# Optimization experiments

Hardware: AMD Instinct MI355X
Metric: run time of the kernel (lower is better)

The kernel has to match this reference:

```python
import jax, jax.numpy as jnp
import numpy as np

N_EMBED = 192
N_HEAD = 6
HEAD_DIM = N_EMBED // N_HEAD  # 32


def setup_inputs() -> dict:
    key = jax.random.key(0)
    k1, k2, k3, k4, k5 = jax.random.split(key, 5)
    B, T = 2048, 128
    scale_qkv = 1.0 / np.sqrt(N_EMBED)
    return {
        "x": jax.random.normal(k1, (B, T, N_EMBED), dtype=jnp.float32),
        "w_qkv": jax.random.normal(k2, (N_EMBED, 3 * N_EMBED), dtype=jnp.float32) * scale_qkv,
        "b_qkv": jax.random.normal(k3, (3 * N_EMBED,), dtype=jnp.float32) * 0.01,
        "w_proj": jax.random.normal(k4, (N_EMBED, N_EMBED), dtype=jnp.float32) * scale_qkv,
        "b_proj": jax.random.normal(k5, (N_EMBED,), dtype=jnp.float32) * 0.01,
    }


def reference(x, w_qkv, b_qkv, w_proj, b_proj):
    B, T, C = x.shape
    qkv = x @ w_qkv + b_qkv                       # [B, T, 3C]
    q, k, v = jnp.split(qkv, 3, axis=-1)
    # [B, H, T, D]
    def heads(t):
        return t.reshape(B, T, N_HEAD, HEAD_DIM).transpose(0, 2, 1, 3)
    q, k, v = heads(q), heads(k), heads(v)
    att = jnp.einsum("bhtd,bhsd->bhts", q, k) / np.sqrt(HEAD_DIM).astype(x.dtype)
    causal = jnp.tril(jnp.ones((T, T), dtype=bool))
    att = jnp.where(causal, att, jnp.finfo(att.dtype).min)
    att = jax.nn.softmax(att, axis=-1)
    # dropout is identity in eval mode
    y = jnp.einsum("bhts,bhsd->bhtd", att, v)      # [B, H, T, D]
    y = y.transpose(0, 2, 1, 3).reshape(B, T, C)
    return y @ w_proj + b_proj
```

## Files before the change

kernel.cpp:

```cpp
#include <hip/hip_runtime.h>
#include <hip/hip_bf16.h>

#define T_  128
#define C_  192
#define H_  6
#define C3_ 576
#define SLAB_ELEMS (96 * 192)
#define SLAB_BYTES (SLAB_ELEMS * 2)

typedef __bf16 bf16x8 __attribute__((ext_vector_type(8)));
typedef __bf16 bf16x4 __attribute__((ext_vector_type(4)));
typedef float  f32x4  __attribute__((ext_vector_type(4)));
typedef unsigned short u16;

__global__ void prep_weights(const float* __restrict__ w_qkv,
                             const float* __restrict__ w_proj,
                             u16* __restrict__ wt)
{
    int idx = blockIdx.x * 256 + threadIdx.x;
    if (idx >= 8 * SLAB_ELEMS) return;
    int slab = idx / SLAB_ELEMS;
    int rem  = idx % SLAB_ELEMS;
    int nl   = rem / 192;
    int kkp  = rem % 192;
    int d    = kkp ^ ((nl & 7) << 3);
    int kt   = d >> 5;
    int e    = d & 31;
    int g    = e >> 3;
    int r    = e & 7;
    int hi   = r >> 2;
    int i    = r & 3;
    int k    = kt * 32 + hi * 16 + g * 4 + i;
    float v;
    if (slab < 6) {
        int sec = nl >> 5;
        int col = sec * C_ + slab * 32 + (nl & 31);
        v = w_qkv[(size_t)k * C3_ + col];
    } else {
        int col = (slab - 6) * 96 + nl;
        v = w_proj[(size_t)k * C_ + col];
    }
    __bf16 bv = (__bf16)v;
    wt[idx] = *reinterpret_cast<u16*>(&bv);
}

__device__ __forceinline__ bf16x8 ld_frag(const __bf16* p) {
    union { bf16x8 v; struct { bf16x4 lo, hi; } s; } u;
    u.s.lo = *reinterpret_cast<const bf16x4*>(p);
    u.s.hi = *reinterpret_cast<const bf16x4*>(p + 16);
    return u.v;
}

__device__ __forceinline__ bf16x8 ld_w(const __bf16* wl, int nl, int kt, int g) {
    return *reinterpret_cast<const bf16x8*>(
        &wl[nl * 192 + (((kt << 5) + (g << 3)) ^ ((nl & 7) << 3))]);
}

__device__ __forceinline__ void stage_slab(const u16* __restrict__ src, u16* dst,
                                           int wid, int lane) {
    #pragma unroll
    for (int p = 0; p < 9; ++p) {
        int off = p * 2048 + wid * 512;
        __builtin_amdgcn_global_load_lds(
            (const __attribute__((address_space(1))) void*)(src + off + lane * 8),
            (__attribute__((address_space(3))) void*)(dst + off), 16, 0, 0);
    }
}

__global__ __launch_bounds__(256, 2) void attn_fused(
    const float* __restrict__ x,
    const u16*   __restrict__ wt,
    const float* __restrict__ b_qkv,
    const float* __restrict__ b_proj,
    float* __restrict__ y)
{
    __shared__ __align__(16) u16   w_lds[SLAB_ELEMS];
    __shared__ __align__(16) __bf16 k_s[128][40];
    __shared__ __align__(16) __bf16 vt_s[32][136];

    const __bf16* wl = reinterpret_cast<const __bf16*>(w_lds);

    const int b    = blockIdx.x;
    const int tid  = threadIdx.x;
    const int wid  = tid >> 6;
    const int lane = tid & 63;
    const int li   = lane & 15;
    const int g    = lane >> 4;

    const float scale = 0.17677669529663687f;

    stage_slab(wt, w_lds, wid, lane);

    bf16x8 xf[2][6];
    #pragma unroll
    for (int m = 0; m < 2; ++m) {
        const float* xr = x + ((size_t)b * T_ + 32*wid + 16*m + li) * C_;
        #pragma unroll
        for (int kt = 0; kt < 6; ++kt) {
            f32x4 a0 = *reinterpret_cast<const f32x4*>(xr + kt*32 + 4*g);
            f32x4 a1 = *reinterpret_cast<const f32x4*>(xr + kt*32 + 16 + 4*g);
            bf16x8 f;
            f[0] = (__bf16)a0[0]; f[1] = (__bf16)a0[1]; f[2] = (__bf16)a0[2]; f[3] = (__bf16)a0[3];
            f[4] = (__bf16)a1[0]; f[5] = (__bf16)a1[1]; f[6] = (__bf16)a1[2]; f[7] = (__bf16)a1[3];
            xf[m][kt] = f;
        }
    }

    bf16x8 of[2][6];

    #pragma unroll
    for (int h = 0; h < H_; ++h) {
        __syncthreads();

        f32x4 qacc[2][2];
        #pragma unroll
        for (int nt = 0; nt < 6; ++nt) {
            const int sec = nt >> 1;
            const int nl  = nt * 16 + li;
            f32x4 bias = *reinterpret_cast<const f32x4*>(
                &b_qkv[sec * C_ + h * 32 + (nt & 1) * 16 + 4 * g]);
            f32x4 acc0 = bias, acc1 = bias;
            #pragma unroll
            for (int kt = 0; kt < 6; ++kt) {
                bf16x8 wf = ld_w(wl, nl, kt, g);
                acc0 = __builtin_amdgcn_mfma_f32_16x16x32_bf16(wf, xf[0][kt], acc0, 0, 0, 0);
                acc1 = __builtin_amdgcn_mfma_f32_16x16x32_bf16(wf, xf[1][kt], acc1, 0, 0, 0);
            }
            if (nt < 2) {
                qacc[0][nt] = acc0;
                qacc[1][nt] = acc1;
            } else if (nt < 4) {
                bf16x4 pk0, pk1;
                #pragma unroll
                for (int j = 0; j < 4; ++j) { pk0[j]=(__bf16)acc0[j]; pk1[j]=(__bf16)acc1[j]; }
                *reinterpret_cast<bf16x4*>(&k_s[32*wid      + li][(nt & 1)*16 + 4*g]) = pk0;
                *reinterpret_cast<bf16x4*>(&k_s[32*wid + 16 + li][(nt & 1)*16 + 4*g]) = pk1;
            } else {
                #pragma unroll
                for (int r = 0; r < 4; ++r) {
                    vt_s[(nt & 1)*16 + 4*g + r][32*wid      + li] = (__bf16)acc0[r];
                    vt_s[(nt & 1)*16 + 4*g + r][32*wid + 16 + li] = (__bf16)acc1[r];
                }
            }
        }
        bf16x8 qf[2];
        #pragma unroll
        for (int m = 0; m < 2; ++m)
            #pragma unroll
            for (int j = 0; j < 4; ++j) {
                qf[m][j]     = (__bf16)(qacc[m][0][j] * scale);
                qf[m][4 + j] = (__bf16)(qacc[m][1][j] * scale);
            }
        __syncthreads();

        stage_slab(wt + (h + 1) * SLAB_ELEMS, w_lds, wid, lane);

        f32x4 lv[2];
        f32x4 oacc[2][2];
        #pragma unroll
        for (int m = 0; m < 2; ++m) {
            lv[m] = f32x4{0.f, 0.f, 0.f, 0.f};
            oacc[m][0] = f32x4{0.f, 0.f, 0.f, 0.f};
            oacc[m][1] = f32x4{0.f, 0.f, 0.f, 0.f};
        }
        #pragma unroll
        for (int hh = 0; hh < 2; ++hh) {
            if (hh == 1 && wid < 2) break;
            f32x4 sacc[2][4];
            #pragma unroll
            for (int j = 0; j < 4; ++j) {
                const int tile = hh*4 + j;
                if (tile > 2*wid + 1) {
                    sacc[0][j] = f32x4{0.f,0.f,0.f,0.f};
                    sacc[1][j] = f32x4{0.f,0.f,0.f,0.f};
                    continue;
                }
                bf16x8 kf = ld_frag(&k_s[tile*16 + li][4*g]);
                f32x4 z = {0.f, 0.f, 0.f, 0.f};
                sacc[0][j] = __builtin_amdgcn_mfma_f32_16x16x32_bf16(kf, qf[0], z, 0, 0, 0);
                sacc[1][j] = __builtin_amdgcn_mfma_f32_16x16x32_bf16(kf, qf[1], z, 0, 0, 0);
            }
            #pragma unroll
            for (int m = 0; m < 2; ++m) {
                const int rt = 2*wid + m;
                #pragma unroll
                for (int j = 0; j < 4; ++j) {
                    const int tile = hh*4 + j;
                    if (tile > rt) {
                        sacc[m][j] = f32x4{0.f,0.f,0.f,0.f};
                    } else if (tile == rt) {
                        #pragma unroll
                        for (int r = 0; r < 4; ++r) {
                            float p = (4*g + r <= li) ? __expf(sacc[m][j][r]) : 0.f;
                            sacc[m][j][r] = p;
                            lv[m][r] += p;
                        }
                    } else {
                        #pragma unroll
                        for (int r = 0; r < 4; ++r) {
                            float p = __expf(sacc[m][j][r]);
                            sacc[m][j][r] = p;
                            lv[m][r] += p;
                        }
                    }
                }
            }
            #pragma unroll
            for (int kp = 0; kp < 2; ++kp) {
                if (hh*4 + 2*kp > 2*wid + 1) break;
                bf16x8 vf0 = ld_frag(&vt_s[li     ][(hh*2 + kp)*32 + 4*g]);
                bf16x8 vf1 = ld_frag(&vt_s[16 + li][(hh*2 + kp)*32 + 4*g]);
                #pragma unroll
                for (int m = 0; m < 2; ++m) {
                    bf16x8 pf;
                    #pragma unroll
                    for (int j2 = 0; j2 < 4; ++j2) {
                        pf[j2]     = (__bf16)sacc[m][2*kp][j2];
                        pf[4 + j2] = (__bf16)sacc[m][2*kp + 1][j2];
                    }
                    oacc[m][0] = __builtin_amdgcn_mfma_f32_16x16x32_bf16(vf0, pf, oacc[m][0], 0, 0, 0);
                    oacc[m][1] = __builtin_amdgcn_mfma_f32_16x16x32_bf16(vf1, pf, oacc[m][1], 0, 0, 0);
                }
            }
        }
        #pragma unroll
        for (int m = 0; m < 2; ++m) {
            float l = (lv[m][0] + lv[m][1]) + (lv[m][2] + lv[m][3]);
            l += __shfl_xor(l, 16);
            l += __shfl_xor(l, 32);
            const float rl = 1.f / l;
            #pragma unroll
            for (int j = 0; j < 4; ++j) {
                of[m][h][j]     = (__bf16)(oacc[m][0][j] * rl);
                of[m][h][4 + j] = (__bf16)(oacc[m][1][j] * rl);
            }
        }
    }

    float* yr = y + (size_t)b * T_ * C_;
    #pragma unroll
    for (int chunk = 0; chunk < 2; ++chunk) {
        __syncthreads();
        #pragma unroll
        for (int nt = 0; nt < 6; ++nt) {
            const int nl = nt * 16 + li;
            f32x4 bias = *reinterpret_cast<const f32x4*>(
                &b_proj[chunk * 96 + nt*16 + 4*g]);
            f32x4 acc0 = bias, acc1 = bias;
            #pragma unroll
            for (int kt = 0; kt < 6; ++kt) {
                bf16x8 wf = ld_w(wl, nl, kt, g);
                acc0 = __builtin_amdgcn_mfma_f32_16x16x32_bf16(wf, of[0][kt], acc0, 0, 0, 0);
                acc1 = __builtin_amdgcn_mfma_f32_16x16x32_bf16(wf, of[1][kt], acc1, 0, 0, 0);
            }
            *reinterpret_cast<f32x4*>(&yr[(size_t)(32*wid      + li) * C_ + chunk*96 + nt*16 + 4*g]) = acc0;
            *reinterpret_cast<f32x4*>(&yr[(size_t)(32*wid + 16 + li) * C_ + chunk*96 + nt*16 + 4*g]) = acc1;
        }
        if (chunk == 0) {
            __syncthreads();
            stage_slab(wt + 7 * SLAB_ELEMS, w_lds, wid, lane);
        }
    }
}

extern "C" void kernel_launch(void* const* d_in, const int* in_sizes, int n_in,
                              void* d_out, int out_size, void* d_ws, size_t ws_size,
                              hipStream_t stream) {
    const float* x      = (const float*)d_in[0];
    const float* w_qkv  = (const float*)d_in[1];
    const float* b_qkv  = (const float*)d_in[2];
    const float* w_proj = (const float*)d_in[3];
    const float* b_proj = (const float*)d_in[4];
    float* yv = (float*)d_out;
    u16*   wt = (u16*)d_ws;
    const int B = in_sizes[0] / (T_ * C_);

    prep_weights<<<(8 * SLAB_ELEMS + 255) / 256, 256, 0, stream>>>(w_qkv, w_proj, wt);
    attn_fused<<<B, 256, 0, stream>>>(x, wt, b_qkv, b_proj, yv);
}
```

Measured before the change: 186.4 us.

## Stream attention in 32-key chunks with exp2 softmax and raise occupancy to 3 waves

Restructures the per-head attention inner loop so that each 32-key chunk computes its scores, exponentiates them and accumulates P·V straight away, rather than holding up to eight score tiles per row block. Folding log2(e) into the Q scale lets exp2f replace __expf, and the row-sum accumulators shrink from vectors to scalars. It also tightens the K and V^T LDS padding and raises launch_bounds from 2 to 3 blocks per SM to increase occupancy. Trade-offs: the smaller padding may cause more LDS bank conflicts, and the higher occupancy target caps registers per thread and could force spills.

```diff
diff --git a/kernel.cpp b/kernel.cpp
--- a/kernel.cpp
+++ b/kernel.cpp
@@ -67,7 +67,7 @@
     }
 }
 
-__global__ __launch_bounds__(256, 2) void attn_fused(
+__global__ __launch_bounds__(256, 3) void attn_fused(
     const float* __restrict__ x,
     const u16*   __restrict__ wt,
     const float* __restrict__ b_qkv,
@@ -75,8 +75,8 @@
     float* __restrict__ y)
 {
     __shared__ __align__(16) u16   w_lds[SLAB_ELEMS];
-    __shared__ __align__(16) __bf16 k_s[128][40];
-    __shared__ __align__(16) __bf16 vt_s[32][136];
+    __shared__ __align__(16) __bf16 k_s[128][36];
+    __shared__ __align__(16) __bf16 vt_s[32][132];
 
     const __bf16* wl = reinterpret_cast<const __bf16*>(w_lds);
 
@@ -87,7 +87,7 @@
     const int li   = lane & 15;
     const int g    = lane >> 4;
 
-    const float scale = 0.17677669529663687f;
+    const float scale2 = 0.25503482459546f;
 
     stage_slab(wt, w_lds, wid, lane);
 
@@ -148,84 +148,68 @@
         for (int m = 0; m < 2; ++m)
             #pragma unroll
             for (int j = 0; j < 4; ++j) {
-                qf[m][j]     = (__bf16)(qacc[m][0][j] * scale);
-                qf[m][4 + j] = (__bf16)(qacc[m][1][j] * scale);
+                qf[m][j]     = (__bf16)(qacc[m][0][j] * scale2);
+                qf[m][4 + j] = (__bf16)(qacc[m][1][j] * scale2);
             }
         __syncthreads();
 
         stage_slab(wt + (h + 1) * SLAB_ELEMS, w_lds, wid, lane);
 
-        f32x4 lv[2];
+        float l0 = 0.f, l1 = 0.f;
         f32x4 oacc[2][2];
         #pragma unroll
         for (int m = 0; m < 2; ++m) {
-            lv[m] = f32x4{0.f, 0.f, 0.f, 0.f};
             oacc[m][0] = f32x4{0.f, 0.f, 0.f, 0.f};
             oacc[m][1] = f32x4{0.f, 0.f, 0.f, 0.f};
         }
         #pragma unroll
-        for (int hh = 0; hh < 2; ++hh) {
-            if (hh == 1 && wid < 2) break;
-            f32x4 sacc[2][4];
+        for (int qq = 0; qq < 4; ++qq) {
+            if (qq > wid) break;
+            bf16x8 kf0 = ld_frag(&k_s[(2*qq    )*16 + li][4*g]);
+            bf16x8 kf1 = ld_frag(&k_s[(2*qq + 1)*16 + li][4*g]);
+            f32x4 z = {0.f, 0.f, 0.f, 0.f};
+            f32x4 s00 = __builtin_amdgcn_mfma_f32_16x16x32_bf16(kf0, qf[0], z, 0, 0, 0);
+            f32x4 s01 = __builtin_amdgcn_mfma_f32_16x16x32_bf16(kf1, qf[0], z, 0, 0, 0);
+            f32x4 s10 = __builtin_amdgcn_mfma_f32_16x16x32_bf16(kf0, qf[1], z, 0, 0, 0);
+            f32x4 s11 = __builtin_amdgcn_mfma_f32_16x16x32_bf16(kf1, qf[1], z, 0, 0, 0);
+            if (qq == wid) {
+                #pragma unroll
+                for (int r = 0; r < 4; ++r) {
+                    float p00 = (4*g + r <= li) ? exp2f(s00[r]) : 0.f;
+                    float p10 = exp2f(s10[r]);
+                    float p11 = (4*g + r <= li) ? exp2f(s11[r]) : 0.f;
+                    s00[r] = p00;  s01[r] = 0.f;  s10[r] = p10;  s11[r] = p11;
+                    l0 += p00;
+                    l1 += p10 + p11;
+                }
+            } else {
+                #pragma unroll
+                for (int r = 0; r < 4; ++r) {
+                    float p00 = exp2f(s00[r]);
+                    float p01 = exp2f(s01[r]);
+                    float p10 = exp2f(s10[r]);
+                    float p11 = exp2f(s11[r]);
+                    s00[r] = p00;  s01[r] = p01;  s10[r] = p10;  s11[r] = p11;
+                    l0 += p00 + p01;
+                    l1 += p10 + p11;
+                }
+            }
+            bf16x8 vf0 = ld_frag(&vt_s[li     ][qq*32 + 4*g]);
+            bf16x8 vf1 = ld_frag(&vt_s[16 + li][qq*32 + 4*g]);
+            bf16x8 pf0, pf1;
             #pragma unroll
             for (int j = 0; j < 4; ++j) {
-                const int tile = hh*4 + j;
-                if (tile > 2*wid + 1) {
-                    sacc[0][j] = f32x4{0.f,0.f,0.f,0.f};
-                    sacc[1][j] = f32x4{0.f,0.f,0.f,0.f};
-                    continue;
-                }
-                bf16x8 kf = ld_frag(&k_s[tile*16 + li][4*g]);
-                f32x4 z = {0.f, 0.f, 0.f, 0.f};
-                sacc[0][j] = __builtin_amdgcn_mfma_f32_16x16x32_bf16(kf, qf[0], z, 0, 0, 0);
-                sacc[1][j] = __builtin_amdgcn_mfma_f32_16x16x32_bf16(kf, qf[1], z, 0, 0, 0);
-            }
-            #pragma unroll
-            for (int m = 0; m < 2; ++m) {
-                const int rt = 2*wid + m;
-                #pragma unroll
-                for (int j = 0; j < 4; ++j) {
-                    const int tile = hh*4 + j;
-                    if (tile > rt) {
-                        sacc[m][j] = f32x4{0.f,0.f,0.f,0.f};
-                    } else if (tile == rt) {
-                        #pragma unroll
-                        for (int r = 0; r < 4; ++r) {
-                            float p = (4*g + r <= li) ? __expf(sacc[m][j][r]) : 0.f;
-                            sacc[m][j][r] = p;
-                            lv[m][r] += p;
-                        }
-                    } else {
-                        #pragma unroll
-                        for (int r = 0; r < 4; ++r) {
-                            float p = __expf(sacc[m][j][r]);
-                            sacc[m][j][r] = p;
-                            lv[m][r] += p;
-                        }
-                    }
-                }
-            }
-            #pragma unroll
-            for (int kp = 0; kp < 2; ++kp) {
-                if (hh*4 + 2*kp > 2*wid + 1) break;
-                bf16x8 vf0 = ld_frag(&vt_s[li     ][(hh*2 + kp)*32 + 4*g]);
-                bf16x8 vf1 = ld_frag(&vt_s[16 + li][(hh*2 + kp)*32 + 4*g]);
-                #pragma unroll
-                for (int m = 0; m < 2; ++m) {
-                    bf16x8 pf;
-                    #pragma unroll
-                    for (int j2 = 0; j2 < 4; ++j2) {
-                        pf[j2]     = (__bf16)sacc[m][2*kp][j2];
-                        pf[4 + j2] = (__bf16)sacc[m][2*kp + 1][j2];
-                    }
-                    oacc[m][0] = __builtin_amdgcn_mfma_f32_16x16x32_bf16(vf0, pf, oacc[m][0], 0, 0, 0);
-                    oacc[m][1] = __builtin_amdgcn_mfma_f32_16x16x32_bf16(vf1, pf, oacc[m][1], 0, 0, 0);
-                }
-            }
+                pf0[j] = (__bf16)s00[j];  pf0[4 + j] = (__bf16)s01[j];
+                pf1[j] = (__bf16)s10[j];  pf1[4 + j] = (__bf16)s11[j];
+            }
+            oacc[0][0] = __builtin_amdgcn_mfma_f32_16x16x32_bf16(vf0, pf0, oacc[0][0], 0, 0, 0);
+            oacc[0][1] = __builtin_amdgcn_mfma_f32_16x16x32_bf16(vf1, pf0, oacc[0][1], 0, 0, 0);
+            oacc[1][0] = __builtin_amdgcn_mfma_f32_16x16x32_bf16(vf0, pf1, oacc[1][0], 0, 0, 0);
+            oacc[1][1] = __builtin_amdgcn_mfma_f32_16x16x32_bf16(vf1, pf1, oacc[1][1], 0, 0, 0);
         }
         #pragma unroll
         for (int m = 0; m < 2; ++m) {
-            float l = (lv[m][0] + lv[m][1]) + (lv[m][2] + lv[m][3]);
+            float l = (m == 0) ? l0 : l1;
             l += __shfl_xor(l, 16);
             l += __shfl_xor(l, 32);
             const float rl = 1.f / l;
```

New measurement: 215.8 us. +15.7%, slower.

## Balance causal attention work across waves by pairing row tiles wid and 7-wid

Applied to the files above, without the earlier changes.

Each wave now owns query row tiles wid and 7-wid instead of two adjacent tiles, so every wave processes the same number of causal key tiles. Before, the last wave did far more attention work than the first. The change also folds log2(e) into the Q scale so exp2f can replace __expf. Register pressure may rise because sacc1 now holds eight tiles, and the rows written by each wave are no longer contiguous.

```diff
diff --git a/kernel.cpp b/kernel.cpp
--- a/kernel.cpp
+++ b/kernel.cpp
@@ -87,14 +87,19 @@
     const int li   = lane & 15;
     const int g    = lane >> 4;
 
-    const float scale = 0.17677669529663687f;
+    const int rt0 = wid;
+    const int rt1 = 7 - wid;
+    const int n1  = rt1;
+
+    const float scale2 = 0.25503482459546f;
 
     stage_slab(wt, w_lds, wid, lane);
 
     bf16x8 xf[2][6];
     #pragma unroll
     for (int m = 0; m < 2; ++m) {
-        const float* xr = x + ((size_t)b * T_ + 32*wid + 16*m + li) * C_;
+        const int row = 16 * (m == 0 ? rt0 : rt1) + li;
+        const float* xr = x + ((size_t)b * T_ + row) * C_;
         #pragma unroll
         for (int kt = 0; kt < 6; ++kt) {
             f32x4 a0 = *reinterpret_cast<const f32x4*>(xr + kt*32 + 4*g);
@@ -133,13 +138,13 @@
                 bf16x4 pk0, pk1;
                 #pragma unroll
                 for (int j = 0; j < 4; ++j) { pk0[j]=(__bf16)acc0[j]; pk1[j]=(__bf16)acc1[j]; }
-                *reinterpret_cast<bf16x4*>(&k_s[32*wid      + li][(nt & 1)*16 + 4*g]) = pk0;
-                *reinterpret_cast<bf16x4*>(&k_s[32*wid + 16 + li][(nt & 1)*16 + 4*g]) = pk1;
+                *reinterpret_cast<bf16x4*>(&k_s[16*rt0 + li][(nt & 1)*16 + 4*g]) = pk0;
+                *reinterpret_cast<bf16x4*>(&k_s[16*rt1 + li][(nt & 1)*16 + 4*g]) = pk1;
             } else {
                 #pragma unroll
                 for (int r = 0; r < 4; ++r) {
-                    vt_s[(nt & 1)*16 + 4*g + r][32*wid      + li] = (__bf16)acc0[r];
-                    vt_s[(nt & 1)*16 + 4*g + r][32*wid + 16 + li] = (__bf16)acc1[r];
+                    vt_s[(nt & 1)*16 + 4*g + r][16*rt0 + li] = (__bf16)acc0[r];
+                    vt_s[(nt & 1)*16 + 4*g + r][16*rt1 + li] = (__bf16)acc1[r];
                 }
             }
         }
@@ -148,91 +153,111 @@
         for (int m = 0; m < 2; ++m)
             #pragma unroll
             for (int j = 0; j < 4; ++j) {
-                qf[m][j]     = (__bf16)(qacc[m][0][j] * scale);
-                qf[m][4 + j] = (__bf16)(qacc[m][1][j] * scale);
+                qf[m][j]     = (__bf16)(qacc[m][0][j] * scale2);
+                qf[m][4 + j] = (__bf16)(qacc[m][1][j] * scale2);
             }
         __syncthreads();
 
         stage_slab(wt + (h + 1) * SLAB_ELEMS, w_lds, wid, lane);
 
-        f32x4 lv[2];
-        f32x4 oacc[2][2];
-        #pragma unroll
-        for (int m = 0; m < 2; ++m) {
-            lv[m] = f32x4{0.f, 0.f, 0.f, 0.f};
-            oacc[m][0] = f32x4{0.f, 0.f, 0.f, 0.f};
-            oacc[m][1] = f32x4{0.f, 0.f, 0.f, 0.f};
-        }
-        #pragma unroll
-        for (int hh = 0; hh < 2; ++hh) {
-            if (hh == 1 && wid < 2) break;
-            f32x4 sacc[2][4];
+        f32x4 sacc0[4], sacc1[8];
+        const f32x4 z = {0.f, 0.f, 0.f, 0.f};
+        #pragma unroll
+        for (int t = 0; t < 8; ++t) {
+            if (t <= n1) {
+                bf16x8 kf = ld_frag(&k_s[t*16 + li][4*g]);
+                sacc1[t] = __builtin_amdgcn_mfma_f32_16x16x32_bf16(kf, qf[1], z, 0, 0, 0);
+                if (t < 4) {
+                    if (t <= wid)
+                        sacc0[t] = __builtin_amdgcn_mfma_f32_16x16x32_bf16(kf, qf[0], z, 0, 0, 0);
+                    else
+                        sacc0[t] = z;
+                }
+            } else {
+                sacc1[t] = z;
+                if (t < 4) sacc0[t] = z;
+            }
+        }
+        f32x4 lv0 = z, lv1 = z;
+        #pragma unroll
+        for (int t = 0; t < 4; ++t) {
+            if (t <= wid) {
+                if (t == wid) {
+                    #pragma unroll
+                    for (int r = 0; r < 4; ++r) {
+                        float p = (4*g + r <= li) ? exp2f(sacc0[t][r]) : 0.f;
+                        sacc0[t][r] = p;  lv0[r] += p;
+                    }
+                } else {
+                    #pragma unroll
+                    for (int r = 0; r < 4; ++r) {
+                        float p = exp2f(sacc0[t][r]);
+                        sacc0[t][r] = p;  lv0[r] += p;
+                    }
+                }
+            }
+        }
+        #pragma unroll
+        for (int t = 0; t < 8; ++t) {
+            if (t <= n1) {
+                if (t == n1) {
+                    #pragma unroll
+                    for (int r = 0; r < 4; ++r) {
+                        float p = (4*g + r <= li) ? exp2f(sacc1[t][r]) : 0.f;
+                        sacc1[t][r] = p;  lv1[r] += p;
+                    }
+                } else {
+                    #pragma unroll
+                    for (int r = 0; r < 4; ++r) {
+                        float p = exp2f(sacc1[t][r]);
+                        sacc1[t][r] = p;  lv1[r] += p;
+                    }
+                }
+            }
+        }
+        f32x4 oacc0[2], oacc1[2];
+        oacc0[0] = z; oacc0[1] = z; oacc1[0] = z; oacc1[1] = z;
+        #pragma unroll
+        for (int p = 0; p < 4; ++p) {
+            if (2*p > n1) break;
+            bf16x8 vf0 = ld_frag(&vt_s[li     ][p*32 + 4*g]);
+            bf16x8 vf1 = ld_frag(&vt_s[16 + li][p*32 + 4*g]);
+            bf16x8 pf1;
             #pragma unroll
             for (int j = 0; j < 4; ++j) {
-                const int tile = hh*4 + j;
-                if (tile > 2*wid + 1) {
-                    sacc[0][j] = f32x4{0.f,0.f,0.f,0.f};
-                    sacc[1][j] = f32x4{0.f,0.f,0.f,0.f};
-                    continue;
-                }
-                bf16x8 kf = ld_frag(&k_s[tile*16 + li][4*g]);
-                f32x4 z = {0.f, 0.f, 0.f, 0.f};
-                sacc[0][j] = __builtin_amdgcn_mfma_f32_16x16x32_bf16(kf, qf[0], z, 0, 0, 0);
-                sacc[1][j] = __builtin_amdgcn_mfma_f32_16x16x32_bf16(kf, qf[1], z, 0, 0, 0);
-            }
-            #pragma unroll
-            for (int m = 0; m < 2; ++m) {
-                const int rt = 2*wid + m;
-                #pragma unroll
-                for (int j = 0; j < 4; ++j) {
-                    const int tile = hh*4 + j;
-                    if (tile > rt) {
-                        sacc[m][j] = f32x4{0.f,0.f,0.f,0.f};
-                    } else if (tile == rt) {
-                        #pragma unroll
-                        for (int r = 0; r < 4; ++r) {
-                            float p = (4*g + r <= li) ? __expf(sacc[m][j][r]) : 0.f;
-                            sacc[m][j][r] = p;
-                            lv[m][r] += p;
-                        }
-                    } else {
-                        #pragma unroll
-                        for (int r = 0; r < 4; ++r) {
-                            float p = __expf(sacc[m][j][r]);
-                            sacc[m][j][r] = p;
-                            lv[m][r] += p;
-                        }
-                    }
-                }
-            }
-            #pragma unroll
-            for (int kp = 0; kp < 2; ++kp) {
-                if (hh*4 + 2*kp > 2*wid + 1) break;
-                bf16x8 vf0 = ld_frag(&vt_s[li     ][(hh*2 + kp)*32 + 4*g]);
-                bf16x8 vf1 = ld_frag(&vt_s[16 + li][(hh*2 + kp)*32 + 4*g]);
-                #pragma unroll
-                for (int m = 0; m < 2; ++m) {
-                    bf16x8 pf;
-                    #pragma unroll
-                    for (int j2 = 0; j2 < 4; ++j2) {
-                        pf[j2]     = (__bf16)sacc[m][2*kp][j2];
-                        pf[4 + j2] = (__bf16)sacc[m][2*kp + 1][j2];
-                    }
-                    oacc[m][0] = __builtin_amdgcn_mfma_f32_16x16x32_bf16(vf0, pf, oacc[m][0], 0, 0, 0);
-                    oacc[m][1] = __builtin_amdgcn_mfma_f32_16x16x32_bf16(vf1, pf, oacc[m][1], 0, 0, 0);
-                }
-            }
-        }
-        #pragma unroll
-        for (int m = 0; m < 2; ++m) {
-            float l = (lv[m][0] + lv[m][1]) + (lv[m][2] + lv[m][3]);
-            l += __shfl_xor(l, 16);
-            l += __shfl_xor(l, 32);
-            const float rl = 1.f / l;
+                pf1[j]     = (__bf16)sacc1[2*p][j];
+                pf1[4 + j] = (__bf16)sacc1[2*p + 1][j];
+            }
+            oacc1[0] = __builtin_amdgcn_mfma_f32_16x16x32_bf16(vf0, pf1, oacc1[0], 0, 0, 0);
+            oacc1[1] = __builtin_amdgcn_mfma_f32_16x16x32_bf16(vf1, pf1, oacc1[1], 0, 0, 0);
+            if (p < 2) {
+                if (2*p <= wid) {
+                    bf16x8 pf0;
+                    #pragma unroll
+                    for (int j = 0; j < 4; ++j) {
+                        pf0[j]     = (__bf16)sacc0[2*p][j];
+                        pf0[4 + j] = (__bf16)sacc0[2*p + 1][j];
+                    }
+                    oacc0[0] = __builtin_amdgcn_mfma_f32_16x16x32_bf16(vf0, pf0, oacc0[0], 0, 0, 0);
+                    oacc0[1] = __builtin_amdgcn_mfma_f32_16x16x32_bf16(vf1, pf0, oacc0[1], 0, 0, 0);
+                }
+            }
+        }
+        {
+            float l0 = (lv0[0] + lv0[1]) + (lv0[2] + lv0[3]);
+            l0 += __shfl_xor(l0, 16);
+            l0 += __shfl_xor(l0, 32);
+            const float rl0 = 1.f / l0;
+            float l1 = (lv1[0] + lv1[1]) + (lv1[2] + lv1[3]);
+            l1 += __shfl_xor(l1, 16);
+            l1 += __shfl_xor(l1, 32);
+            const float rl1 = 1.f / l1;
             #pragma unroll
             for (int j = 0; j < 4; ++j) {
-                of[m][h][j]     = (__bf16)(oacc[m][0][j] * rl);
-                of[m][h][4 + j] = (__bf16)(oacc[m][1][j] * rl);
+                of[0][h][j]     = (__bf16)(oacc0[0][j] * rl0);
+                of[0][h][4 + j] = (__bf16)(oacc0[1][j] * rl0);
+                of[1][h][j]     = (__bf16)(oacc1[0][j] * rl1);
+                of[1][h][4 + j] = (__bf16)(oacc1[1][j] * rl1);
             }
         }
     }
@@ -253,8 +278,8 @@
                 acc0 = __builtin_amdgcn_mfma_f32_16x16x32_bf16(wf, of[0][kt], acc0, 0, 0, 0);
                 acc1 = __builtin_amdgcn_mfma_f32_16x16x32_bf16(wf, of[1][kt], acc1, 0, 0, 0);
             }
-            *reinterpret_cast<f32x4*>(&yr[(size_t)(32*wid      + li) * C_ + chunk*96 + nt*16 + 4*g]) = acc0;
-            *reinterpret_cast<f32x4*>(&yr[(size_t)(32*wid + 16 + li) * C_ + chunk*96 + nt*16 + 4*g]) = acc1;
+            *reinterpret_cast<f32x4*>(&yr[(size_t)(16*rt0 + li) * C_ + chunk*96 + nt*16 + 4*g]) = acc0;
+            *reinterpret_cast<f32x4*>(&yr[(size_t)(16*rt1 + li) * C_ + chunk*96 + nt*16 + 4*g]) = acc1;
         }
         if (chunk == 0) {
             __syncthreads();
```

Result: slower. 195.3 us (+4.7%).
